# Optimization experiments

Measured on AMD Instinct MI355X. Metric: run time of the kernel, lower is better.

The kernel has to match this reference:

```python
import jax, jax.numpy as jnp
import numpy as np

B, C, D, H, W = 4, 64, 32, 64, 64
S, NH = 8, 4
HD = C // NH


def setup_inputs() -> dict:
    key = jax.random.key(0)
    ks = jax.random.split(key, 8)
    sc = 0.05
    return {
        "x": jax.random.normal(ks[0], (B, C, D, H, W), jnp.float32),
        "slot_init": jax.random.normal(ks[1], (1, C, S), jnp.float32),
        "slot_proj_w": jax.random.normal(ks[2], (C, C), jnp.float32) * sc,
        "slot_proj_b": jnp.zeros((C,), jnp.float32),
        "ln_g": jnp.ones((C,), jnp.float32),
        "ln_b": jnp.zeros((C,), jnp.float32),
        "in_proj_w": jax.random.normal(ks[3], (3 * C, C), jnp.float32) * sc,
        "in_proj_b": jnp.zeros((3 * C,), jnp.float32),
        "out_proj_w": jax.random.normal(ks[4], (C, C), jnp.float32) * sc,
        "out_proj_b": jnp.zeros((C,), jnp.float32),
        "feat_w": jax.random.normal(ks[5], (C, C), jnp.float32) * sc,
        "feat_b": jnp.zeros((C,), jnp.float32),
        "s2f_w": jax.random.normal(ks[6], (C, C), jnp.float32) * sc,
        "s2f_b": jnp.zeros((C,), jnp.float32),
    }


def _l2norm(v, axis):
    # F.normalize: v / max(||v||, eps)
    n = jnp.sqrt(jnp.sum(v * v, axis=axis, keepdims=True))
    return v / jnp.maximum(n, 1e-12)


def reference(x, slot_init, slot_proj_w, slot_proj_b, ln_g, ln_b,
              in_proj_w, in_proj_b, out_proj_w, out_proj_b,
              feat_w, feat_b, s2f_w, s2f_b):
    b, c, d, h, w = x.shape
    n = d * h * w
    x_flat = x.reshape(b, c, n)                                  # (b,c,N)
    slots = jnp.broadcast_to(slot_init, (b, c, S))               # (b,c,S)

    # ---- slot update: cosine-sim cross attention over N ----
    x_norm = _l2norm(x_flat, 1)
    slots_norm = _l2norm(slots, 1)
    sim = jnp.einsum('bcs,bcn->bsn', slots_norm, x_norm)         # (b,S,N)
    attn = jax.nn.softmax(sim, axis=2)
    updates = jnp.einsum('bcn,bsn->bsc', x_flat, attn)           # (b,S,c)
    slots_t = updates @ slot_proj_w.T + slot_proj_b              # (b,S,c)

    # ---- LayerNorm(channels) then tiny MHSA over S=8 slots ----
    mu = jnp.mean(slots_t, axis=-1, keepdims=True)
    var = jnp.mean((slots_t - mu) ** 2, axis=-1, keepdims=True)
    sn = (slots_t - mu) / jnp.sqrt(var + 1e-5) * ln_g + ln_b     # (b,S,c)

    qkv = sn @ in_proj_w.T + in_proj_b                           # (b,S,3c)
    q, k, v = jnp.split(qkv, 3, axis=-1)
    def heads(t):
        return t.reshape(b, S, NH, HD).transpose(0, 2, 1, 3)     # (b,H,S,hd)
    q, k, v = heads(q), heads(k), heads(v)
    scores = jnp.einsum('bhqd,bhkd->bhqk', q, k) / jnp.sqrt(jnp.float32(HD))
    a = jax.nn.softmax(scores, axis=-1)
    o = jnp.einsum('bhqk,bhkd->bhqd', a, v).transpose(0, 2, 1, 3).reshape(b, S, c)
    o = o @ out_proj_w.T + out_proj_b
    slots_t = slots_t + o                                        # (b,S,c)

    # ---- feature broadcast: 1x1x1 conv + slot->feature attention ----
    feat_flat = jnp.einsum('oc,bcn->bon', feat_w, x_flat) + feat_b[None, :, None]
    slots_feat = slots_t @ s2f_w.T + s2f_b                       # (b,S,c)
    sim2 = jnp.einsum('bsc,bcn->bsn', slots_feat, feat_flat)
    attn2 = jax.nn.softmax(sim2, axis=1)                         # softmax over slots
    out = jnp.einsum('bsc,bsn->bcn', slots_t, attn2)             # (b,c,N)
    return out.reshape(b, c, d, h, w) + x
```

## Files before the change

### kernel.cpp

```cpp
#include <hip/hip_runtime.h>
#include <hip/hip_bf16.h>

#define BB   4
#define CC   64
#define SS   8
#define NN   (32*64*64)
#define NH_  4
#define HD_  16
#define TA   128
#define BPA  256
#define NB1  256
#define NTB2 4

typedef __attribute__((ext_vector_type(8))) short bf16x8;
typedef __attribute__((ext_vector_type(4))) float f32x4;

__device__ __forceinline__ float b2f(unsigned short h) {
    union { unsigned u; float f; } v; v.u = ((unsigned)h) << 16; return v.f;
}
__device__ __forceinline__ unsigned bfpack(float a, float b) {
    union { float f; unsigned u; } x, y; x.f = a; y.f = b;
    unsigned ra = (x.u + 0x7FFFu + ((x.u >> 16) & 1u)) >> 16;
    unsigned rb = (y.u + 0x7FFFu + ((y.u >> 16) & 1u)) & 0xFFFF0000u;
    return ra | rb;
}

__global__ __launch_bounds__(256) void k_precomp(
    const float* __restrict__ slot_init,
    const float* __restrict__ s2fw, const float* __restrict__ s2fb,
    const float* __restrict__ fw, const float* __restrict__ fb,
    float* __restrict__ M, float* __restrict__ g0v,
    float* __restrict__ hv, float* __restrict__ h0,
    float* __restrict__ snT_ws)
{
    const int tid = threadIdx.x;
    if (blockIdx.x < 16) {
        const int cp = blockIdx.x*4 + (tid >> 6);
        const int c  = tid & 63;
        float acc = 0.f;
        #pragma unroll 8
        for (int o = 0; o < CC; ++o)
            acc += s2fw[o*CC + cp] * fw[o*CC + c];
        M[cp*CC + c] = acc;
    } else if (blockIdx.x == 16) {
        if (tid < 64) {
            float acc = 0.f;
            #pragma unroll 8
            for (int o = 0; o < CC; ++o) acc += s2fb[o] * fw[o*CC + tid];
            g0v[tid] = acc;
        } else if (tid < 128) {
            const int cp = tid - 64;
            float acc = 0.f;
            #pragma unroll 8
            for (int o = 0; o < CC; ++o) acc += s2fw[o*CC + cp] * fb[o];
            hv[cp] = acc;
        } else if (tid == 128) {
            float acc = 0.f;
            for (int o = 0; o < CC; ++o) acc += s2fb[o] * fb[o];
            *h0 = acc;
        }
    } else {
        __shared__ float nrm[SS];
        if (tid < 64) {
            const int s = tid & 7, ch = tid >> 3;
            float p = 0.f;
            #pragma unroll
            for (int j = 0; j < 8; ++j) {
                float v = slot_init[(ch*8 + j)*SS + s];
                p += v*v;
            }
            p += __shfl_xor(p, 8); p += __shfl_xor(p, 16); p += __shfl_xor(p, 32);
            if (tid < 8) nrm[s] = fmaxf(sqrtf(p), 1e-12f);
        }
        __syncthreads();
        for (int i = tid; i < SS*CC; i += 256) {
            const int c = i >> 3, s = i & 7;
            snT_ws[i] = slot_init[c*SS + s] / nrm[s];
        }
    }
}

__global__ __launch_bounds__(256) void k_sim(
    const float* __restrict__ x, const float* __restrict__ snT_ws,
    unsigned short* __restrict__ xb16, unsigned short* __restrict__ ebf,
    float* __restrict__ sume_part)
{
    __shared__ float snT[CC*SS];
    __shared__ float red[SS*256];

    const int tid  = threadIdx.x;
    const int b    = blockIdx.x >> 8;
    const int blk1 = blockIdx.x & 255;
    const int n    = (((blk1 << 8) + tid)) * 2;

    if (tid < 128) *(float4*)&snT[tid*4] = *(const float4*)&snT_ws[tid*4];
    __syncthreads();

    const float* xcol = x + (size_t)b*CC*NN + n;
    unsigned short* xo = xb16 + (size_t)b*CC*NN + n;

    float ss0 = 0.f, ss1 = 0.f;
    float a0[SS], a1[SS];
    #pragma unroll
    for (int s = 0; s < SS; ++s) { a0[s] = 0.f; a1[s] = 0.f; }

    #pragma unroll
    for (int c = 0; c < CC; ++c) {
        const float2 xv = *(const float2*)(xcol + (size_t)c*NN);
        *(unsigned*)(xo + (size_t)c*NN) = bfpack(xv.x, xv.y);
        ss0 += xv.x*xv.x;  ss1 += xv.y*xv.y;
        const float4 g0 = *(const float4*)&snT[c*8];
        const float4 g1 = *(const float4*)&snT[c*8 + 4];
        a0[0] += g0.x*xv.x; a0[1] += g0.y*xv.x; a0[2] += g0.z*xv.x; a0[3] += g0.w*xv.x;
        a0[4] += g1.x*xv.x; a0[5] += g1.y*xv.x; a0[6] += g1.z*xv.x; a0[7] += g1.w*xv.x;
        a1[0] += g0.x*xv.y; a1[1] += g0.y*xv.y; a1[2] += g0.z*xv.y; a1[3] += g0.w*xv.y;
        a1[4] += g1.x*xv.y; a1[5] += g1.y*xv.y; a1[6] += g1.z*xv.y; a1[7] += g1.w*xv.y;
    }

    const float i0 = 1.f / fmaxf(sqrtf(ss0), 1e-12f);
    const float i1 = 1.f / fmaxf(sqrtf(ss1), 1e-12f);
    unsigned short* eo = ebf + (size_t)b*SS*NN + n;
    float esum[SS];
    #pragma unroll
    for (int s = 0; s < SS; ++s) {
        const float e0 = __expf(a0[s] * i0);
        const float e1 = __expf(a1[s] * i1);
        *(unsigned*)(eo + (size_t)s*NN) = bfpack(e0, e1);
        esum[s] = e0 + e1;
    }

    #pragma unroll
    for (int s = 0; s < SS; ++s) red[s*256 + tid] = esum[s];
    __syncthreads();
    {
        const int s = tid >> 5, j = tid & 31;
        float v = 0.f;
        #pragma unroll
        for (int k = 0; k < 8; ++k) v += red[s*256 + j*8 + k];
        v += __shfl_xor(v, 1); v += __shfl_xor(v, 2); v += __shfl_xor(v, 4);
        v += __shfl_xor(v, 8); v += __shfl_xor(v, 16);
        if (j == 0) sume_part[(size_t)(b*NB1 + blk1)*SS + s] = v;
    }
}

__global__ __launch_bounds__(256) void k_gemm_u(
    const unsigned short* __restrict__ xb16, const unsigned short* __restrict__ ebf,
    float* __restrict__ U_part)
{
    __shared__ short xt[2][CC*TA];
    __shared__ short et[2][SS*TA];
    __shared__ short etz[TA];

    const int tid = threadIdx.x;
    const int b   = blockIdx.x / BPA;
    const int blk = blockIdx.x % BPA;
    const int lane = tid & 63, wv = tid >> 6;

    if (tid < 64) ((int*)etz)[tid] = 0;

    const unsigned short* xg = xb16 + (size_t)b*CC*NN;
    const unsigned short* eg = ebf  + (size_t)b*SS*NN;

    f32x4 accU = {0.f, 0.f, 0.f, 0.f};

    #define STG(buf, t)                                                        \
    {                                                                          \
        const int n0_ = (t) * TA;                                              \
        _Pragma("unroll")                                                      \
        for (int k = 0; k < 4; ++k) {                                          \
            const int c_ = wv*16 + k*4 + (lane >> 4);                          \
            const int j_ = (lane & 15) ^ (c_ & 7);                             \
            const unsigned short* src_ = xg + (size_t)c_*NN + n0_ + j_*8;      \
            short* dst_ = &xt[buf][(wv*16 + k*4)*TA];                          \
            __builtin_amdgcn_global_load_lds(                                  \
                (const __attribute__((address_space(1))) void*)src_,           \
                (__attribute__((address_space(3))) void*)dst_, 16, 0, 0);      \
        }                                                                      \
        if (wv == 0) {                                                         \
            _Pragma("unroll")                                                  \
            for (int k = 0; k < 2; ++k) {                                      \
                const int s_ = k*4 + (lane >> 4);                              \
                const int j_ = (lane & 15) ^ (s_ & 7);                         \
                const unsigned short* src_ = eg + (size_t)s_*NN + n0_ + j_*8;  \
                short* dst_ = &et[buf][k*4*TA];                                \
                __builtin_amdgcn_global_load_lds(                              \
                    (const __attribute__((address_space(1))) void*)src_,       \
                    (__attribute__((address_space(3))) void*)dst_, 16, 0, 0);  \
            }                                                                  \
        }                                                                      \
    }

    int cur = 0;
    STG(0, blk);
    asm volatile("s_waitcnt vmcnt(0)" ::: "memory");
    __syncthreads();

    for (int tt = 0; tt < NTB2; ++tt) {
        if (tt + 1 < NTB2) STG(cur ^ 1, blk + (tt+1)*BPA);

        {
            const int ca  = (wv << 4) + (lane & 15);
            const int rbq = lane & 15;
            const int p   = lane >> 4;
            const short* brow = (rbq < 8) ? &et[cur][rbq*TA] : etz;
            const int bsw = (rbq < 8) ? (rbq & 7) : 0;
            #pragma unroll
            for (int kk = 0; kk < 4; ++kk) {
                const int sl = kk*4 + p;
                const bf16x8 af  = *(const bf16x8*)&xt[cur][ca*TA + ((sl ^ (ca & 7)) << 3)];
                const bf16x8 bfr = *(const bf16x8*)&brow[(sl ^ bsw) << 3];
                accU = __builtin_amdgcn_mfma_f32_16x16x32_bf16(af, bfr, accU, 0, 0, 0);
            }
        }
        asm volatile("s_waitcnt vmcnt(0)" ::: "memory");
        __syncthreads();
        cur ^= 1;
    }
    #undef STG

    {
        const size_t base = ((size_t)(b*BPA + blk) * SS) * CC;
        if ((lane & 15) < SS) {
            const int s  = lane & 15;
            const int c0 = (wv << 4) + ((lane >> 4) << 2);
            #pragma unroll
            for (int r = 0; r < 4; ++r)
                U_part[base + s*CC + c0 + r] = accU[r];
        }
    }
}

__global__ __launch_bounds__(256) void k_reduce2(
    const float* __restrict__ U_part, const float* __restrict__ sume_part,
    float* __restrict__ upd_g, int nU, int nL)
{
    __shared__ float part[4][64];
    __shared__ float lbuf[256];
    __shared__ float Lsh;
    const int tid = threadIdx.x;
    const int b = blockIdx.x >> 3, s = blockIdx.x & 7;
    const int c = tid & 63, kc = tid >> 6;
    const int cnt = nU >> 2;

    float lv = 0.f;
    for (int k = tid; k < nL; k += 256)
        lv += sume_part[(size_t)(b*nL + k)*SS + s];
    lbuf[tid] = lv;

    float acc[8];
    #pragma unroll
    for (int j = 0; j < 8; ++j) acc[j] = 0.f;
    const float* base = U_part + ((size_t)(b*nU + kc*cnt)*SS + s)*CC + c;
    for (int k = 0; k < cnt; k += 8) {
        #pragma unroll
        for (int j = 0; j < 8; ++j)
            acc[j] += base[(size_t)(k + j) * SS * CC];
    }
    part[kc][c] = ((acc[0]+acc[1]) + (acc[2]+acc[3]))
                + ((acc[4]+acc[5]) + (acc[6]+acc[7]));
    __syncthreads();

    if (tid < 128) lbuf[tid] += lbuf[tid + 128];
    __syncthreads();
    if (tid < 64) {
        float v = lbuf[tid] + lbuf[tid + 64];
        v += __shfl_xor(v, 1); v += __shfl_xor(v, 2); v += __shfl_xor(v, 4);
        v += __shfl_xor(v, 8); v += __shfl_xor(v, 16); v += __shfl_xor(v, 32);
        if (tid == 0) Lsh = v;
    }
    __syncthreads();

    if (tid < 64) {
        float u = part[0][c] + part[1][c] + part[2][c] + part[3][c];
        upd_g[((size_t)b*SS + s)*CC + c] = u / Lsh;
    }
}

__global__ __launch_bounds__(256) void k_slots_small(
    const float* __restrict__ upd_g,
    const float* __restrict__ spw, const float* __restrict__ spb,
    const float* __restrict__ lng, const float* __restrict__ lnb,
    const float* __restrict__ ipw, const float* __restrict__ ipb,
    const float* __restrict__ opw, const float* __restrict__ opb,
    const float* __restrict__ M, const float* __restrict__ g0v,
    const float* __restrict__ hv, const float* __restrict__ h0,
    float* __restrict__ st_out, float* __restrict__ g_out, float* __restrict__ h_out)
{
    __shared__ float upd[SS*CC];
    __shared__ float st [SS*CC];
    __shared__ float snb[SS*CC];
    __shared__ float qkv[SS*3*CC];
    __shared__ float ot [SS*CC];

    const int tid  = threadIdx.x;
    const int b    = blockIdx.x;
    const int c    = tid & 63;
    const int quad = tid >> 6;
    const int r0 = quad*2, r1 = r0 + 1;
    float wreg[CC];

    #pragma unroll
    for (int i = 0; i < 16; ++i)
        *(float4*)&wreg[i*4] = *(const float4*)(spw + c*CC + i*4);
    upd[r0*CC + c] = upd_g[(b*SS + r0)*CC + c];
    upd[r1*CC + c] = upd_g[(b*SS + r1)*CC + c];
    __syncthreads();

    {
        const float bias = spb[c];
        float a0 = bias, a1 = bias;
        #pragma unroll
        for (int i = 0; i < 16; ++i) {
            float4 u0 = *(const float4*)&upd[r0*CC + i*4];
            float4 u1 = *(const float4*)&upd[r1*CC + i*4];
            a0 += u0.x*wreg[i*4+0] + u0.y*wreg[i*4+1] + u0.z*wreg[i*4+2] + u0.w*wreg[i*4+3];
            a1 += u1.x*wreg[i*4+0] + u1.y*wreg[i*4+1] + u1.z*wreg[i*4+2] + u1.w*wreg[i*4+3];
        }
        st[r0*CC + c] = a0;
        st[r1*CC + c] = a1;
    }
    __syncthreads();

    {
        const int row = tid >> 5, l = tid & 31;
        float v0 = st[row*CC + l], v1 = st[row*CC + l + 32];
        float sum = v0 + v1;
        sum += __shfl_xor(sum, 1); sum += __shfl_xor(sum, 2); sum += __shfl_xor(sum, 4);
        sum += __shfl_xor(sum, 8); sum += __shfl_xor(sum, 16);
        const float mu = sum * (1.f/64.f);
        const float d0 = v0 - mu, d1 = v1 - mu;
        float vs = d0*d0 + d1*d1;
        vs += __shfl_xor(vs, 1); vs += __shfl_xor(vs, 2); vs += __shfl_xor(vs, 4);
        vs += __shfl_xor(vs, 8); vs += __shfl_xor(vs, 16);
        const float rstd = rsqrtf(vs * (1.f/64.f) + 1e-5f);
        snb[row*CC + l]      = d0 * rstd * lng[l]      + lnb[l];
        snb[row*CC + l + 32] = d1 * rstd * lng[l + 32] + lnb[l + 32];
    }
    __syncthreads();

    for (int m = 0; m < 3; ++m) {
        #pragma unroll
        for (int i = 0; i < 16; ++i)
            *(float4*)&wreg[i*4] = *(const float4*)(ipw + (size_t)(m*CC + c)*CC + i*4);
        const float bias = ipb[m*CC + c];
        float a0 = bias, a1 = bias;
        #pragma unroll
        for (int i = 0; i < 16; ++i) {
            float4 u0 = *(const float4*)&snb[r0*CC + i*4];
            float4 u1 = *(const float4*)&snb[r1*CC + i*4];
            a0 += u0.x*wreg[i*4+0] + u0.y*wreg[i*4+1] + u0.z*wreg[i*4+2] + u0.w*wreg[i*4+3];
            a1 += u1.x*wreg[i*4+0] + u1.y*wreg[i*4+1] + u1.z*wreg[i*4+2] + u1.w*wreg[i*4+3];
        }
        qkv[r0*3*CC + m*CC + c] = a0;
        qkv[r1*3*CC + m*CC + c] = a1;
    }
    __syncthreads();

    if (tid < NH_*SS) {
        const int h = tid >> 3, q = tid & 7;
        float qreg[HD_];
        #pragma unroll
        for (int i = 0; i < 4; ++i)
            *(float4*)&qreg[i*4] = *(const float4*)&qkv[q*3*CC + h*HD_ + i*4];
        float srow[SS];
        float mx = -1e30f;
        #pragma unroll
        for (int k = 0; k < SS; ++k) {
            float acc = 0.f;
            #pragma unroll
            for (int d = 0; d < HD_; ++d)
                acc += qreg[d] * qkv[k*3*CC + CC + h*HD_ + d];
            srow[k] = acc * 0.25f;
            mx = fmaxf(mx, srow[k]);
        }
        float l = 0.f;
        #pragma unroll
        for (int k = 0; k < SS; ++k) { srow[k] = __expf(srow[k] - mx); l += srow[k]; }
        const float inv = 1.f / l;
        float oreg[HD_];
        #pragma unroll
        for (int d = 0; d < HD_; ++d) oreg[d] = 0.f;
        #pragma unroll
        for (int k = 0; k < SS; ++k) {
            #pragma unroll
            for (int d = 0; d < HD_; ++d)
                oreg[d] += srow[k] * qkv[k*3*CC + 2*CC + h*HD_ + d];
        }
        #pragma unroll
        for (int d = 0; d < HD_; ++d)
            ot[q*CC + h*HD_ + d] = oreg[d] * inv;
    }
    __syncthreads();

    #pragma unroll
    for (int i = 0; i < 16; ++i)
        *(float4*)&wreg[i*4] = *(const float4*)(opw + c*CC + i*4);
    {
        const float bias = opb[c];
        float a0 = bias, a1 = bias;
        #pragma unroll
        for (int i = 0; i < 16; ++i) {
            float4 u0 = *(const float4*)&ot[r0*CC + i*4];
            float4 u1 = *(const float4*)&ot[r1*CC + i*4];
            a0 += u0.x*wreg[i*4+0] + u0.y*wreg[i*4+1] + u0.z*wreg[i*4+2] + u0.w*wreg[i*4+3];
            a1 += u1.x*wreg[i*4+0] + u1.y*wreg[i*4+1] + u1.z*wreg[i*4+2] + u1.w*wreg[i*4+3];
        }
        st[r0*CC + c] += a0;
        st[r1*CC + c] += a1;
    }
    __syncthreads();

    #pragma unroll 8
    for (int cp = 0; cp < CC; ++cp) wreg[cp] = M[cp*CC + c];
    {
        const float g0 = g0v[c];
        float a0 = g0, a1 = g0;
        #pragma unroll
        for (int i = 0; i < 16; ++i) {
            float4 s0 = *(const float4*)&st[r0*CC + i*4];
            float4 s1 = *(const float4*)&st[r1*CC + i*4];
            a0 += s0.x*wreg[i*4+0] + s0.y*wreg[i*4+1] + s0.z*wreg[i*4+2] + s0.w*wreg[i*4+3];
            a1 += s1.x*wreg[i*4+0] + s1.y*wreg[i*4+1] + s1.z*wreg[i*4+2] + s1.w*wreg[i*4+3];
        }
        g_out[(b*SS + r0)*CC + c] = a0;
        g_out[(b*SS + r1)*CC + c] = a1;
        st_out[(b*SS + r0)*CC + c] = st[r0*CC + c];
        st_out[(b*SS + r1)*CC + c] = st[r1*CC + c];
    }
    {
        const int row = tid >> 5, l = tid & 31;
        float pv = st[row*CC + l]*hv[l] + st[row*CC + l + 32]*hv[l + 32];
        pv += __shfl_xor(pv, 1); pv += __shfl_xor(pv, 2); pv += __shfl_xor(pv, 4);
        pv += __shfl_xor(pv, 8); pv += __shfl_xor(pv, 16);
        if (l == 0) h_out[b*SS + row] = pv + *h0;
    }
}

__global__ __launch_bounds__(256) void k_feat(
    const unsigned short* __restrict__ xb16,
    const float* __restrict__ st_g, const float* __restrict__ g_g,
    const float* __restrict__ h_g,
    float* __restrict__ out)
{
    __shared__ float stS[SS*CC];
    __shared__ float gS [SS*CC];
    __shared__ float hS [SS];

    const int tid = threadIdx.x;
    const int b  = blockIdx.x >> 8;
    const int n  = (((blockIdx.x & 255) << 8) + tid) * 2;

    for (int i = tid; i < SS*CC; i += 256) {
        stS[i] = st_g[b*SS*CC + i];
        gS[i]  = g_g [b*SS*CC + i];
    }
    if (tid < SS) hS[tid] = h_g[b*SS + tid];
    __syncthreads();

    const unsigned short* xbh = xb16 + (size_t)b*CC*NN + n;

    float a0[SS], a1[SS];
    #pragma unroll
    for (int s = 0; s < SS; ++s) { a0[s] = hS[s]; a1[s] = hS[s]; }
    #pragma unroll
    for (int c4 = 0; c4 < CC/4; ++c4) {
        float lo[4], hi[4];
        #pragma unroll
        for (int j = 0; j < 4; ++j) {
            const unsigned u = *(const unsigned*)(xbh + (size_t)(c4*4 + j)*NN);
            lo[j] = b2f((unsigned short)(u & 0xFFFFu));
            hi[j] = b2f((unsigned short)(u >> 16));
        }
        #pragma unroll
        for (int s = 0; s < SS; ++s) {
            const float4 g4 = *(const float4*)(&gS[s*CC + c4*4]);
            a0[s] += g4.x*lo[0] + g4.y*lo[1] + g4.z*lo[2] + g4.w*lo[3];
            a1[s] += g4.x*hi[0] + g4.y*hi[1] + g4.z*hi[2] + g4.w*hi[3];
        }
    }

    float m0 = a0[0], m1 = a1[0];
    #pragma unroll
    for (int s = 1; s < SS; ++s) { m0 = fmaxf(m0, a0[s]); m1 = fmaxf(m1, a1[s]); }
    float l0 = 0.f, l1 = 0.f;
    #pragma unroll
    for (int s = 0; s < SS; ++s) {
        a0[s] = __expf(a0[s] - m0); l0 += a0[s];
        a1[s] = __expf(a1[s] - m1); l1 += a1[s];
    }
    const float inv0 = 1.f / l0, inv1 = 1.f / l1;
    #pragma unroll
    for (int s = 0; s < SS; ++s) { a0[s] *= inv0; a1[s] *= inv1; }

    float* ob = out + (size_t)b * CC * NN + n;
    #pragma unroll
    for (int c4 = 0; c4 < CC/4; ++c4) {
        float p0[4] = {0.f, 0.f, 0.f, 0.f};
        float p1[4] = {0.f, 0.f, 0.f, 0.f};
        #pragma unroll
        for (int s = 0; s < SS; ++s) {
            const float4 s4 = *(const float4*)(&stS[s*CC + c4*4]);
            p0[0] += s4.x*a0[s]; p0[1] += s4.y*a0[s]; p0[2] += s4.z*a0[s]; p0[3] += s4.w*a0[s];
            p1[0] += s4.x*a1[s]; p1[1] += s4.y*a1[s]; p1[2] += s4.z*a1[s]; p1[3] += s4.w*a1[s];
        }
        #pragma unroll
        for (int j = 0; j < 4; ++j) {
            const int c = c4*4 + j;
            const unsigned u = *(const unsigned*)(xbh + (size_t)c*NN);
            float2 o;
            o.x = p0[j] + b2f((unsigned short)(u & 0xFFFFu));
            o.y = p1[j] + b2f((unsigned short)(u >> 16));
            *(float2*)(ob + (size_t)c*NN) = o;
        }
    }
}

extern "C" void kernel_launch(void* const* d_in, const int* in_sizes, int n_in,
                              void* d_out, int out_size, void* d_ws, size_t ws_size,
                              hipStream_t stream) {
    const float* x         = (const float*)d_in[0];
    const float* slot_init = (const float*)d_in[1];
    const float* spw       = (const float*)d_in[2];
    const float* spb       = (const float*)d_in[3];
    const float* lng       = (const float*)d_in[4];
    const float* lnb       = (const float*)d_in[5];
    const float* ipw       = (const float*)d_in[6];
    const float* ipb       = (const float*)d_in[7];
    const float* opw       = (const float*)d_in[8];
    const float* opb       = (const float*)d_in[9];
    const float* fw        = (const float*)d_in[10];
    const float* fb        = (const float*)d_in[11];
    const float* s2fw      = (const float*)d_in[12];
    const float* s2fb      = (const float*)d_in[13];
    float* out = (float*)d_out;

    float* w         = (float*)d_ws;
    float* U_part    = w;
    float* sume_part = U_part + (size_t)BB*BPA*SS*CC;
    float* upd_g     = sume_part + (size_t)BB*NB1*SS;
    float* Mm        = upd_g + 2048;
    float* g0v       = Mm + 4096;
    float* hv        = g0v + 64;
    float* h0        = hv + 64;
    float* snT_ws    = h0 + 64;
    float* st_out    = snT_ws + 1024;
    float* g_out     = st_out + 2048;
    float* h_out     = g_out + 2048;
    unsigned short* xb16 = (unsigned short*)(h_out + 64);
    unsigned short* ebf  = xb16 + (size_t)BB*CC*NN;

    k_precomp<<<18, 256, 0, stream>>>(slot_init, s2fw, s2fb, fw, fb,
                                      Mm, g0v, hv, h0, snT_ws);
    k_sim<<<BB * NB1, 256, 0, stream>>>(x, snT_ws, xb16, ebf, sume_part);
    k_gemm_u<<<BB * BPA, 256, 0, stream>>>(xb16, ebf, U_part);
    k_reduce2<<<BB * SS, 256, 0, stream>>>(U_part, sume_part, upd_g, BPA, NB1);
    k_slots_small<<<BB, 256, 0, stream>>>(upd_g, spw, spb, lng, lnb,
                                          ipw, ipb, opw, opb, Mm, g0v, hv, h0,
                                          st_out, g_out, h_out);
    k_feat<<<BB * NB1, 256, 0, stream>>>(xb16, st_out, g_out, h_out, out);
}
```

Measured before the change: 137.1 us.

## Read fp32 x directly in feature kernel, cache column in registers, nontemporal stores

The feature-broadcast kernel now reads the original fp32 input instead of the bf16 copy, and handles one spatial position per thread instead of two. The 64 channel values are kept in registers so the residual add needs no second read of x. Output is written with nontemporal stores to avoid polluting the cache. This doubles the bytes read from x compared with bf16 but halves the number of passes over it, and the residual now uses exact fp32 x. Holding 64 floats per thread raises register pressure.

```diff
diff --git a/kernel.cpp b/kernel.cpp
--- a/kernel.cpp
+++ b/kernel.cpp
@@ -437,7 +437,7 @@
 }
 
 __global__ __launch_bounds__(256) void k_feat(
-    const unsigned short* __restrict__ xb16,
+    const float* __restrict__ x,
     const float* __restrict__ st_g, const float* __restrict__ g_g,
     const float* __restrict__ h_g,
     float* __restrict__ out)
@@ -447,8 +447,8 @@
     __shared__ float hS [SS];
 
     const int tid = threadIdx.x;
-    const int b  = blockIdx.x >> 8;
-    const int n  = (((blockIdx.x & 255) << 8) + tid) * 2;
+    const int b  = blockIdx.x >> 9;
+    const int n  = ((blockIdx.x & 511) << 8) + tid;
 
     for (int i = tid; i < SS*CC; i += 256) {
         stS[i] = st_g[b*SS*CC + i];
@@ -457,61 +457,50 @@
     if (tid < SS) hS[tid] = h_g[b*SS + tid];
     __syncthreads();
 
-    const unsigned short* xbh = xb16 + (size_t)b*CC*NN + n;
-
-    float a0[SS], a1[SS];
-    #pragma unroll
-    for (int s = 0; s < SS; ++s) { a0[s] = hS[s]; a1[s] = hS[s]; }
+    const float* xcol = x + (size_t)b * CC * NN + n;
+
+    float xc[CC];
+    float a[SS];
+    #pragma unroll
+    for (int s = 0; s < SS; ++s) a[s] = hS[s];
+
     #pragma unroll
     for (int c4 = 0; c4 < CC/4; ++c4) {
-        float lo[4], hi[4];
-        #pragma unroll
-        for (int j = 0; j < 4; ++j) {
-            const unsigned u = *(const unsigned*)(xbh + (size_t)(c4*4 + j)*NN);
-            lo[j] = b2f((unsigned short)(u & 0xFFFFu));
-            hi[j] = b2f((unsigned short)(u >> 16));
-        }
+        #pragma unroll
+        for (int j = 0; j < 4; ++j)
+            xc[c4*4 + j] = xcol[(size_t)(c4*4 + j) * NN];
         #pragma unroll
         for (int s = 0; s < SS; ++s) {
             const float4 g4 = *(const float4*)(&gS[s*CC + c4*4]);
-            a0[s] += g4.x*lo[0] + g4.y*lo[1] + g4.z*lo[2] + g4.w*lo[3];
-            a1[s] += g4.x*hi[0] + g4.y*hi[1] + g4.z*hi[2] + g4.w*hi[3];
-        }
-    }
-
-    float m0 = a0[0], m1 = a1[0];
-    #pragma unroll
-    for (int s = 1; s < SS; ++s) { m0 = fmaxf(m0, a0[s]); m1 = fmaxf(m1, a1[s]); }
-    float l0 = 0.f, l1 = 0.f;
-    #pragma unroll
-    for (int s = 0; s < SS; ++s) {
-        a0[s] = __expf(a0[s] - m0); l0 += a0[s];
-        a1[s] = __expf(a1[s] - m1); l1 += a1[s];
-    }
-    const float inv0 = 1.f / l0, inv1 = 1.f / l1;
-    #pragma unroll
-    for (int s = 0; s < SS; ++s) { a0[s] *= inv0; a1[s] *= inv1; }
+            a[s] += g4.x*xc[c4*4+0] + g4.y*xc[c4*4+1]
+                  + g4.z*xc[c4*4+2] + g4.w*xc[c4*4+3];
+        }
+    }
+
+    float m = a[0];
+    #pragma unroll
+    for (int s = 1; s < SS; ++s) m = fmaxf(m, a[s]);
+    float l = 0.f;
+    #pragma unroll
+    for (int s = 0; s < SS; ++s) { a[s] = __expf(a[s] - m); l += a[s]; }
+    const float inv = 1.f / l;
+    #pragma unroll
+    for (int s = 0; s < SS; ++s) a[s] *= inv;
 
     float* ob = out + (size_t)b * CC * NN + n;
     #pragma unroll
     for (int c4 = 0; c4 < CC/4; ++c4) {
-        float p0[4] = {0.f, 0.f, 0.f, 0.f};
-        float p1[4] = {0.f, 0.f, 0.f, 0.f};
+        float o0 = 0.f, o1 = 0.f, o2 = 0.f, o3 = 0.f;
         #pragma unroll
         for (int s = 0; s < SS; ++s) {
             const float4 s4 = *(const float4*)(&stS[s*CC + c4*4]);
-            p0[0] += s4.x*a0[s]; p0[1] += s4.y*a0[s]; p0[2] += s4.z*a0[s]; p0[3] += s4.w*a0[s];
-            p1[0] += s4.x*a1[s]; p1[1] += s4.y*a1[s]; p1[2] += s4.z*a1[s]; p1[3] += s4.w*a1[s];
-        }
-        #pragma unroll
-        for (int j = 0; j < 4; ++j) {
-            const int c = c4*4 + j;
-            const unsigned u = *(const unsigned*)(xbh + (size_t)c*NN);
-            float2 o;
-            o.x = p0[j] + b2f((unsigned short)(u & 0xFFFFu));
-            o.y = p1[j] + b2f((unsigned short)(u >> 16));
-            *(float2*)(ob + (size_t)c*NN) = o;
-        }
+            o0 += s4.x * a[s]; o1 += s4.y * a[s];
+            o2 += s4.z * a[s]; o3 += s4.w * a[s];
+        }
+        __builtin_nontemporal_store(o0 + xc[c4*4+0], ob + (size_t)(c4*4+0) * NN);
+        __builtin_nontemporal_store(o1 + xc[c4*4+1], ob + (size_t)(c4*4+1) * NN);
+        __builtin_nontemporal_store(o2 + xc[c4*4+2], ob + (size_t)(c4*4+2) * NN);
+        __builtin_nontemporal_store(o3 + xc[c4*4+3], ob + (size_t)(c4*4+3) * NN);
     }
 }
 
@@ -557,5 +546,5 @@
     k_slots_small<<<BB, 256, 0, stream>>>(upd_g, spw, spb, lng, lnb,
                                           ipw, ipb, opw, opb, Mm, g0v, hv, h0,
                                           st_out, g_out, h_out);
-    k_feat<<<BB * NB1, 256, 0, stream>>>(xb16, st_out, g_out, h_out, out);
-}
+    k_feat<<<BB * (NN/256), 256, 0, stream>>>(x, st_out, g_out, h_out, out);
+}
```

Measured after the change: 138.3 us. About the same (+0.9%).
